# Kernel tuning notes

Measured on AMD Instinct MI355X. Metric: run time of the kernel, lower is better.

The kernel has to match this reference:

```python
import jax, jax.numpy as jnp
import numpy as np


def setup_inputs() -> dict:
    key = jax.random.key(0)
    x = jax.random.normal(key, (8, 48, 48, 48, 64), dtype=jnp.float32)
    gamma = jnp.float32(1e-4)  # matches tf.Variable(0.0001)
    return {"x": x, "gamma": gamma}


def reference(x, gamma):
    # x: (B, W, D, H, C)
    B, W, D, H, C = x.shape
    N = W * D * H
    # Keras Reshape((C, -1)) is a row-major flatten of (W, D, H, C) -> (C, N).
    # NOTE: this is NOT a channels-first transpose; it is a raw reshape,
    # exactly as the original module computes it.
    K = x.reshape(B, C, N)                      # (B, C, N)
    # Q = K^T and J = K^T in the original, so m1 = K@Q and m2 = K@J are both
    # the same Gram matrix G = K @ K^T. Compute it once.
    G = jnp.einsum('bcn,bdn->bcd', K, K)        # (B, C, C)
    m3 = jnp.einsum('bcd,bde->bce', G, G)       # (B, C, C)
    affinity = jax.nn.sigmoid(m3)               # (B, C, C)
    weights = jnp.einsum('bcd,bdn->bcn', affinity, K)  # (B, C, N)
    weights = weights.reshape(B, W, D, H, C)
    return gamma * weights + x
```

## Files before the change

### kernel.cpp

```cpp
#include <hip/hip_runtime.h>

#define NCOL 110592
#define NCH  64
#define CN   (NCOL * NCH)
#define NB   8

typedef __attribute__((ext_vector_type(8))) __bf16 bf16x8;
typedef __attribute__((ext_vector_type(4))) float  f32x4;

__global__ __launch_bounds__(256) void k_gram(const float* __restrict__ x,
                                              float* __restrict__ part,
                                              int steps) {
    const int b     = blockIdx.y;
    const int chunk = blockIdx.x;
    const int tid   = threadIdx.x;
    const int w     = tid >> 6;
    const int lane  = tid & 63;
    const int r     = lane & 15;
    const int q     = lane >> 4;

    const float* xb = x + (size_t)b * CN;

    f32x4 acc0 = {0.f, 0.f, 0.f, 0.f};
    f32x4 acc1 = {0.f, 0.f, 0.f, 0.f};
    f32x4 acc2 = {0.f, 0.f, 0.f, 0.f};
    f32x4 acc3 = {0.f, 0.f, 0.f, 0.f};

    const int kbase = chunk * steps * 32 + q * 8;

    for (int s = 0; s < steps; ++s) {
        const int k0 = kbase + s * 32;
        bf16x8 frag[4];
#pragma unroll
        for (int i = 0; i < 4; ++i) {
            const float* p = xb + (i * 16 + r) * NCOL + k0;
            f32x4 lo = *(const f32x4*)p;
            f32x4 hi = *(const f32x4*)(p + 4);
            bf16x8 f;
            f[0] = (__bf16)lo[0]; f[1] = (__bf16)lo[1];
            f[2] = (__bf16)lo[2]; f[3] = (__bf16)lo[3];
            f[4] = (__bf16)hi[0]; f[5] = (__bf16)hi[1];
            f[6] = (__bf16)hi[2]; f[7] = (__bf16)hi[3];
            frag[i] = f;
        }
        bf16x8 af = (w == 0) ? frag[0] : (w == 1) ? frag[1]
                  : (w == 2) ? frag[2] : frag[3];
        acc0 = __builtin_amdgcn_mfma_f32_16x16x32_bf16(af, frag[0], acc0, 0, 0, 0);
        acc1 = __builtin_amdgcn_mfma_f32_16x16x32_bf16(af, frag[1], acc1, 0, 0, 0);
        acc2 = __builtin_amdgcn_mfma_f32_16x16x32_bf16(af, frag[2], acc2, 0, 0, 0);
        acc3 = __builtin_amdgcn_mfma_f32_16x16x32_bf16(af, frag[3], acc3, 0, 0, 0);
    }

    float* pp = part + (size_t)(b * gridDim.x + chunk) * 4096;
#pragma unroll
    for (int rr = 0; rr < 4; ++rr) {
        const int m = w * 16 + q * 4 + rr;
        pp[m * 64 + (0 * 16 + r)] = acc0[rr];
        pp[m * 64 + (1 * 16 + r)] = acc1[rr];
        pp[m * 64 + (2 * 16 + r)] = acc2[rr];
        pp[m * 64 + (3 * 16 + r)] = acc3[rr];
    }
}

__global__ __launch_bounds__(256) void k_reduce(const float* __restrict__ part,
                                                float* __restrict__ G,
                                                int chunks) {
    const int b    = blockIdx.y;
    const int cell = blockIdx.x * 512 + threadIdx.x;
    float s0 = 0.f, s1 = 0.f;
    for (int p = 0; p < chunks; ++p) {
        const float* pp = part + (size_t)(b * chunks + p) * 4096;
        s0 += pp[cell];
        s1 += pp[cell + 256];
    }
    G[b * 4096 + cell]       = s0;
    G[b * 4096 + cell + 256] = s1;
}

__global__ __launch_bounds__(256) void k_affinity(const float* __restrict__ G,
                                                  const float* __restrict__ gptr,
                                                  float* __restrict__ A) {
    const int b = blockIdx.x;
    __shared__ float Gs[64 * 65];
    const float* Gb = G + b * 4096;
    for (int i = threadIdx.x; i < 4096; i += 256)
        Gs[(i >> 6) * 65 + (i & 63)] = Gb[i];
    __syncthreads();
    const float gamma = gptr[0];
    for (int id = threadIdx.x; id < 4096; id += 256) {
        const int c = id >> 6, e = id & 63;
        float dot = 0.f;
#pragma unroll
        for (int d = 0; d < 64; ++d)
            dot += Gs[c * 65 + d] * Gs[e * 65 + d];
        const float aff = 1.0f / (1.0f + __expf(-dot));
        A[b * 4096 + id] = gamma * aff + ((c == e) ? 1.0f : 0.0f);
    }
}

__global__ __launch_bounds__(256) void k_apply(const float* __restrict__ x,
                                               const float* __restrict__ A,
                                               float* __restrict__ out) {
    const int b  = blockIdx.y;
    const int n0 = blockIdx.x * 512 + threadIdx.x;
    const float* xb = x + (size_t)b * CN;
    float*       ob = out + (size_t)b * CN;
    const float* Ab = A + b * 4096;

    float acc0[64], acc1[64];
#pragma unroll
    for (int c = 0; c < 64; ++c) { acc0[c] = 0.f; acc1[c] = 0.f; }

#pragma unroll 4
    for (int d = 0; d < 64; ++d) {
        const float k0 = xb[d * NCOL + n0];
        const float k1 = xb[d * NCOL + n0 + 256];
#pragma unroll
        for (int c = 0; c < 64; ++c) {
            const float a = Ab[d * 64 + c];
            acc0[c] += a * k0;
            acc1[c] += a * k1;
        }
    }

#pragma unroll
    for (int c = 0; c < 64; ++c) {
        ob[c * NCOL + n0]       = acc0[c];
        ob[c * NCOL + n0 + 256] = acc1[c];
    }
}

extern "C" void kernel_launch(void* const* d_in, const int* in_sizes, int n_in,
                              void* d_out, int out_size, void* d_ws, size_t ws_size,
                              hipStream_t stream) {
    const float* x    = (const float*)d_in[0];
    const float* gptr = (const float*)d_in[1];
    float*       out  = (float*)d_out;
    float*       ws   = (float*)d_ws;

    int chunks = 64;
    auto need = [](int ch) { return (size_t)(8 * ch + 16) * 4096 * 4; };
    if (ws_size < need(64)) chunks = 32;
    if (ws_size < need(32)) chunks = 8;
    if (ws_size < need(8))  chunks = 2;
    const int steps = 3456 / chunks;

    float* part = ws;
    float* G    = ws + (size_t)8 * chunks * 4096;
    float* Aff  = G + 8 * 4096;

    k_gram    <<<dim3(chunks, 8), 256, 0, stream>>>(x, part, steps);
    k_reduce  <<<dim3(8, 8),      256, 0, stream>>>(part, G, chunks);
    k_affinity<<<8,               256, 0, stream>>>(G, gptr, Aff);
    k_apply   <<<dim3(216, 8),    256, 0, stream>>>(x, Aff, out);
}
```

Measured before the change: 531.9 us.

## Compute apply stage with bf16 MFMA and add residual separately

The apply kernel moves from a scalar FP32 64x64 matrix product per column, which needs 128 accumulators per thread, to bf16 MFMA tiles. The affinity matrix is now stored as bf16 gamma*sigmoid without the identity term, and the fp32 residual x is added exactly in the epilogue. The gram kernel's chunk count also rises to 128 for more parallelism, and one index is widened to size_t. The cost is bf16 rounding of both the affinity and x in the correction term, and an extra re-read of x for the residual.

```diff
diff --git a/kernel.cpp b/kernel.cpp
--- a/kernel.cpp
+++ b/kernel.cpp
@@ -33,7 +33,7 @@
         bf16x8 frag[4];
 #pragma unroll
         for (int i = 0; i < 4; ++i) {
-            const float* p = xb + (i * 16 + r) * NCOL + k0;
+            const float* p = xb + (size_t)(i * 16 + r) * NCOL + k0;
             f32x4 lo = *(const f32x4*)p;
             f32x4 hi = *(const f32x4*)(p + 4);
             bf16x8 f;
@@ -79,7 +79,7 @@
 
 __global__ __launch_bounds__(256) void k_affinity(const float* __restrict__ G,
                                                   const float* __restrict__ gptr,
-                                                  float* __restrict__ A) {
+                                                  __bf16* __restrict__ S) {
     const int b = blockIdx.x;
     __shared__ float Gs[64 * 65];
     const float* Gb = G + b * 4096;
@@ -94,39 +94,65 @@
         for (int d = 0; d < 64; ++d)
             dot += Gs[c * 65 + d] * Gs[e * 65 + d];
         const float aff = 1.0f / (1.0f + __expf(-dot));
-        A[b * 4096 + id] = gamma * aff + ((c == e) ? 1.0f : 0.0f);
+        S[b * 4096 + id] = (__bf16)(gamma * aff);
     }
 }
 
 __global__ __launch_bounds__(256) void k_apply(const float* __restrict__ x,
-                                               const float* __restrict__ A,
+                                               const __bf16* __restrict__ S,
                                                float* __restrict__ out) {
-    const int b  = blockIdx.y;
-    const int n0 = blockIdx.x * 512 + threadIdx.x;
-    const float* xb = x + (size_t)b * CN;
-    float*       ob = out + (size_t)b * CN;
-    const float* Ab = A + b * 4096;
+    const int b    = blockIdx.y;
+    const int tid  = threadIdx.x;
+    const int w    = tid >> 6;
+    const int lane = tid & 63;
+    const int r    = lane & 15;
+    const int q    = lane >> 4;
 
-    float acc0[64], acc1[64];
+    const float*  xb = x + (size_t)b * CN;
+    float*        ob = out + (size_t)b * CN;
+    const __bf16* Sb = S + b * 4096;
+
+    bf16x8 a[4][2];
 #pragma unroll
-    for (int c = 0; c < 64; ++c) { acc0[c] = 0.f; acc1[c] = 0.f; }
+    for (int ct = 0; ct < 4; ++ct)
+#pragma unroll
+        for (int kh = 0; kh < 2; ++kh)
+            a[ct][kh] = *(const bf16x8*)(Sb + (ct * 16 + r) * 64 + kh * 32 + q * 8);
 
-#pragma unroll 4
-    for (int d = 0; d < 64; ++d) {
-        const float k0 = xb[d * NCOL + n0];
-        const float k1 = xb[d * NCOL + n0 + 256];
+    const int nbase = blockIdx.x * 256 + w * 16 + r;
+
+#pragma unroll 2
+    for (int it = 0; it < 4; ++it) {
+        const int n = nbase + it * 64;
+
+        bf16x8 bfr[2];
 #pragma unroll
-        for (int c = 0; c < 64; ++c) {
-            const float a = Ab[d * 64 + c];
-            acc0[c] += a * k0;
-            acc1[c] += a * k1;
+        for (int kh = 0; kh < 2; ++kh) {
+            const float* p = xb + (size_t)(kh * 32 + q * 8) * NCOL + n;
+            bf16x8 f;
+#pragma unroll
+            for (int j = 0; j < 8; ++j)
+                f[j] = (__bf16)p[(size_t)j * NCOL];
+            bfr[kh] = f;
         }
-    }
+
+        f32x4 acc[4];
+#pragma unroll
+        for (int ct = 0; ct < 4; ++ct) {
+            f32x4 z = {0.f, 0.f, 0.f, 0.f};
+            z = __builtin_amdgcn_mfma_f32_16x16x32_bf16(a[ct][0], bfr[0], z, 0, 0, 0);
+            z = __builtin_amdgcn_mfma_f32_16x16x32_bf16(a[ct][1], bfr[1], z, 0, 0, 0);
+            acc[ct] = z;
+        }
 
 #pragma unroll
-    for (int c = 0; c < 64; ++c) {
-        ob[c * NCOL + n0]       = acc0[c];
-        ob[c * NCOL + n0 + 256] = acc1[c];
+        for (int ct = 0; ct < 4; ++ct) {
+#pragma unroll
+            for (int rr = 0; rr < 4; ++rr) {
+                const size_t o = (size_t)(ct * 16 + q * 4 + rr) * NCOL + n;
+                ob[o] = xb[o] + acc[ct][rr];
+            }
+        }
     }
 }
 
@@ -138,19 +164,20 @@
     float*       out  = (float*)d_out;
     float*       ws   = (float*)d_ws;
 
-    int chunks = 64;
-    auto need = [](int ch) { return (size_t)(8 * ch + 16) * 4096 * 4; };
-    if (ws_size < need(64)) chunks = 32;
-    if (ws_size < need(32)) chunks = 8;
-    if (ws_size < need(8))  chunks = 2;
+    int chunks = 128;
+    auto need = [](int ch) { return (size_t)(8 * ch + 8) * 4096 * 4 + 8 * 4096 * 2; };
+    if (ws_size < need(128)) chunks = 64;
+    if (ws_size < need(64))  chunks = 32;
+    if (ws_size < need(32))  chunks = 8;
+    if (ws_size < need(8))   chunks = 2;
     const int steps = 3456 / chunks;
 
-    float* part = ws;
-    float* G    = ws + (size_t)8 * chunks * 4096;
-    float* Aff  = G + 8 * 4096;
+    float*  part = ws;
+    float*  G    = ws + (size_t)8 * chunks * 4096;
+    __bf16* S    = (__bf16*)(G + 8 * 4096);
 
     k_gram    <<<dim3(chunks, 8), 256, 0, stream>>>(x, part, steps);
     k_reduce  <<<dim3(8, 8),      256, 0, stream>>>(part, G, chunks);
-    k_affinity<<<8,               256, 0, stream>>>(G, gptr, Aff);
-    k_apply   <<<dim3(216, 8),    256, 0, stream>>>(x, Aff, out);
+    k_affinity<<<8,               256, 0, stream>>>(G, gptr, S);
+    k_apply   <<<dim3(432, 8),    256, 0, stream>>>(x, S, out);
 }
```

Result: slower. 580.1 us (+9.1%).
